# Kernel tuning notes

Measured on AMD Instinct MI355X. Metric: run time of the kernel, lower is better.

Reference implementation:

```python
import jax, jax.numpy as jnp
import numpy as np
import math

B = 8
M = 64
A = 3
NUM_CLASSES = 80
IMG = 608
REDUCTIONS = (8.0, 16.0, 32.0)
XY_SCALES = (1.2, 1.1, 1.05)
IOU_THRESH = 0.213
IGNORE_THRESH = 0.7
COORD_SCALE = 0.07
OBJ_SCALE = 1.0
NOOBJ_SCALE = 1.0
CLASS_SCALE = 1.0
BASE_ANCHORS = np.array([[12,16],[19,36],[40,28],[36,75],[76,55],[72,146],[142,110],[192,243],[459,401]], np.float32)
MASKS = [[0,1,2],[3,4,5],[6,7,8]]
ANCHORS = [jnp.asarray(BASE_ANCHORS[m] / r) for m, r in zip(MASKS, REDUCTIONS)]


def _softplus(x):
    return jnp.logaddexp(x, 0.0)


def _bce_logits(x, t):
    # == sum-reduction BCELoss(sigmoid(x), t), elementwise (stable logits form)
    return _softplus(x) - x * t


def _corners(b):
    x1 = b[..., 0] - b[..., 2] * 0.5
    y1 = b[..., 1] - b[..., 3] * 0.5
    x2 = b[..., 0] + b[..., 2] * 0.5
    y2 = b[..., 1] + b[..., 3] * 0.5
    return x1, y1, x2, y2


def _iou_plain(b1, b2):
    # broadcastable xywh boxes -> plain IoU (matches YOLOLoss.iou with iou_type='iou')
    b1x1, b1y1, b1x2, b1y2 = _corners(b1)
    b2x1, b2y1, b2x2, b2y2 = _corners(b2)
    inter = jnp.clip(jnp.minimum(b1x2, b2x2) - jnp.maximum(b1x1, b2x1), 0) * \
            jnp.clip(jnp.minimum(b1y2, b2y2) - jnp.maximum(b1y1, b2y1), 0)
    union = b1[..., 2] * b1[..., 3] + b2[..., 2] * b2[..., 3] + 1e-16 - inter
    return inter / union


def _ciou(b1, b2):
    # elementwise CIoU (matches YOLOLoss.iou_loss with iou_type='ciou')
    b1x1, b1y1, b1x2, b1y2 = _corners(b1)
    b2x1, b2y1, b2x2, b2y2 = _corners(b2)
    inter = jnp.clip(jnp.minimum(b1x2, b2x2) - jnp.maximum(b1x1, b2x1), 0) * \
            jnp.clip(jnp.minimum(b1y2, b2y2) - jnp.maximum(b1y1, b2y1), 0)
    union = b1[..., 2] * b1[..., 3] + b2[..., 2] * b2[..., 3] + 1e-16 - inter
    iou = inter / union
    cw = jnp.maximum(b1x2, b2x2) - jnp.minimum(b1x1, b2x1)
    ch = jnp.maximum(b1y2, b2y2) - jnp.minimum(b1y1, b2y1)
    c2 = cw ** 2 + ch ** 2 + 1e-16
    rho2 = (b1[..., 0] - b2[..., 0]) ** 2 + (b1[..., 1] - b2[..., 1]) ** 2
    v = (4.0 / math.pi ** 2) * (jnp.arctan(b2[..., 2] / b2[..., 3]) - jnp.arctan(b1[..., 2] / b1[..., 3])) ** 2
    alpha = jax.lax.stop_gradient(v / (1.0 - iou + v + 1e-16))
    return iou - (rho2 / c2 + v * alpha)


def _level_loss(pred, targets, cats, anchor, reduction, xy_scale):
    b, c, h, w = pred.shape
    p = pred.reshape(b, A, NUM_CLASSES + 5, h, w).transpose(0, 1, 3, 4, 2)  # [B,A,H,W,85]
    box_xy = jax.nn.sigmoid(p[..., :2]) * xy_scale - 0.5 * (xy_scale - 1.0)
    box_wh = jnp.exp(p[..., 2:4]) * anchor[None, :, None, None, :]
    obj_logit = p[..., 4]
    cls_logit = p[..., 5:]

    tb = targets[:, :4] / reduction           # [M,4] x1y1x2y2 in grid units
    t_bid = targets[:, 4].astype(jnp.int32)   # image index per target
    wh = tb[:, 2:] - tb[:, :2]                # [M,2]

    # wh_iou anchor<->target matching; match = (iou > thresh) | one_hot(best_anchor)
    a_area = anchor[:, 0] * anchor[:, 1]
    t_area = wh[:, 0] * wh[:, 1]
    inter = jnp.minimum(anchor[:, 0][:, None], wh[:, 0][None, :]) * \
            jnp.minimum(anchor[:, 1][:, None], wh[:, 1][None, :])
    iou_at = inter / (a_area[:, None] + t_area[None, :] - inter)   # [A,M]
    best = jnp.argmax(iou_at, axis=0)                              # [M]
    match = (iou_at > IOU_THRESH) | (jnp.arange(A)[:, None] == best[None, :])  # [A,M]
    matchT = match.T.astype(pred.dtype)                            # [M,A]

    cxcy = (tb[:, :2] + tb[:, 2:]) * 0.5
    ij = cxcy.astype(jnp.int32)
    txy = cxcy - ij.astype(pred.dtype)
    ti, tj = ij[:, 0], ij[:, 1]
    tbox = jnp.concatenate([txy, wh], axis=1)                      # [M,4]

    bI = t_bid[:, None]
    aI = jnp.arange(A)[None, :]
    jI = tj[:, None]
    iI = ti[:, None]
    g_box = jnp.concatenate([box_xy[bI, aI, jI, iI], box_wh[bI, aI, jI, iI]], -1)  # [M,A,4]

    ciou = _ciou(g_box, tbox[:, None, :])                          # [M,A]
    iou_loss = jnp.sum(matchT * (1.0 - ciou)) * COORD_SCALE

    # full decoded boxes with grid offsets (square grids: ys=row, xs=col as in source)
    gx = jnp.arange(w, dtype=pred.dtype)[None, :]
    gy = jnp.arange(h, dtype=pred.dtype)[:, None]
    full_box = jnp.stack([box_xy[..., 0] + gx, box_xy[..., 1] + gy,
                          box_wh[..., 0], box_wh[..., 1]], axis=-1)  # [B,A,H,W,4]

    t_xywh = jnp.concatenate([cxcy, wh], axis=1)                   # [M,4]
    iou_full = _iou_plain(full_box[..., None, :], t_xywh)          # [B,A,H,W,M]
    valid = t_bid[None, None, None, None, :] == jnp.arange(b)[:, None, None, None, None]
    ignore = jnp.any((iou_full > IGNORE_THRESH) & valid, axis=-1)  # [B,A,H,W]
    neg = jnp.where(ignore, 0.0, 1.0).astype(pred.dtype)
    neg = neg.at[bI, aI, jI, iI].min(jnp.where(match.T, 0.0, 1.0).astype(pred.dtype))

    g_obj = obj_logit[bI, aI, jI, iI]                              # [M,A]
    obj_pos = jnp.sum(matchT * _bce_logits(g_obj, 1.0))
    obj_neg = jnp.sum(neg * _softplus(obj_logit))
    obj_loss = OBJ_SCALE * obj_pos + NOOBJ_SCALE * obj_neg

    g_cls = cls_logit[bI, aI, jI, iI]                              # [M,A,nc]
    onehot = jax.nn.one_hot(cats - 1, NUM_CLASSES, dtype=pred.dtype)  # [M,nc]
    cls_loss = jnp.sum(matchT * jnp.sum(_bce_logits(g_cls, onehot[:, None, :]), -1)) * CLASS_SCALE

    return iou_loss, obj_loss, cls_loss


def setup_inputs() -> dict:
    key = jax.random.key(0)
    k = jax.random.split(key, 9)
    pred0 = jax.random.normal(k[0], (B, A * (NUM_CLASSES + 5), 76, 76), jnp.float32)
    pred1 = jax.random.normal(k[1], (B, A * (NUM_CLASSES + 5), 38, 38), jnp.float32)
    pred2 = jax.random.normal(k[2], (B, A * (NUM_CLASSES + 5), 19, 19), jnp.float32)
    cx = jax.random.uniform(k[3], (M,), jnp.float32, 16.0, 592.0)
    cy = jax.random.uniform(k[4], (M,), jnp.float32, 16.0, 592.0)
    bw = jax.random.uniform(k[5], (M,), jnp.float32, 8.0, 120.0)
    bh = jax.random.uniform(k[6], (M,), jnp.float32, 8.0, 120.0)
    bid = jax.random.randint(k[7], (M,), 0, B).astype(jnp.float32)
    targets = jnp.stack([cx - bw * 0.5, cy - bh * 0.5, cx + bw * 0.5, cy + bh * 0.5, bid], axis=1)
    cats = jax.random.randint(k[8], (M,), 1, NUM_CLASSES + 1, jnp.int32)
    return {"pred0": pred0, "pred1": pred1, "pred2": pred2, "targets": targets, "cats": cats}


def reference(pred0, pred1, pred2, targets, cats):
    iou_l = obj_l = cls_l = 0.0
    for pred, anchor, red, xys in zip((pred0, pred1, pred2), ANCHORS, REDUCTIONS, XY_SCALES):
        il, ol, cl = _level_loss(pred, targets, cats, anchor, red, xys)
        iou_l = iou_l + il
        obj_l = obj_l + ol
        cls_l = cls_l + cl
    return jnp.stack([iou_l, obj_l, cls_l])  # (iou_loss, obj_loss, cls_loss)
```

## Files before the change

kernel.cpp:

```cpp
#include <hip/hip_runtime.h>
#include <math.h>

#define NCLS 80
#define NA   3
#define NT   64
#define NB   8


__device__ __forceinline__ float sigm(float x) {
    return __builtin_amdgcn_rcpf(1.f + __expf(-x));
}
__device__ __forceinline__ float softplus_f(float x) {
    return fmaxf(x, 0.f) + __logf(1.f + __expf(-fabsf(x)));
}

template <int LVL>
__device__ __forceinline__ void lvl_consts(float& invred, float& xys, float& bias,
                                           float (&aw)[3], float (&ah)[3]) {
    if (LVL == 0) {
        invred = 0.125f;   xys = 1.2f;
        aw[0] = 1.5f;    aw[1] = 2.375f; aw[2] = 5.0f;
        ah[0] = 2.0f;    ah[1] = 4.5f;   ah[2] = 3.5f;
    } else if (LVL == 1) {
        invred = 0.0625f;  xys = 1.1f;
        aw[0] = 2.25f;   aw[1] = 4.75f;  aw[2] = 4.5f;
        ah[0] = 4.6875f; ah[1] = 3.4375f;ah[2] = 9.125f;
    } else {
        invred = 0.03125f; xys = 1.05f;
        aw[0] = 4.4375f; aw[1] = 6.0f;   aw[2] = 14.34375f;
        ah[0] = 3.4375f; ah[1] = 7.59375f; ah[2] = 12.53125f;
    }
    bias = 0.5f * (xys - 1.f);
}

template <int LVL>
__device__ __forceinline__ void load_target(const float* __restrict__ tgt, int t,
                                            float& x1, float& y1, float& x2, float& y2,
                                            float& w, float& h, float& cx, float& cy,
                                            int& ti, int& tj, int& bid, int& mask) {
    float invred, xys, bias, aw[3], ah[3];
    lvl_consts<LVL>(invred, xys, bias, aw, ah);
    x1 = tgt[t * 5 + 0] * invred;
    y1 = tgt[t * 5 + 1] * invred;
    x2 = tgt[t * 5 + 2] * invred;
    y2 = tgt[t * 5 + 3] * invred;
    bid = (int)tgt[t * 5 + 4];
    w = x2 - x1; h = y2 - y1;
    cx = (x1 + x2) * 0.5f; cy = (y1 + y2) * 0.5f;
    ti = (int)cx; tj = (int)cy;
    float ta = w * h;
    float iou[3];
#pragma unroll
    for (int a = 0; a < 3; a++) {
        float inter = fminf(aw[a], w) * fminf(ah[a], h);
        iou[a] = inter / (aw[a] * ah[a] + ta - inter);
    }
    int best = 0;
    if (iou[1] > iou[best]) best = 1;
    if (iou[2] > iou[best]) best = 2;
    mask = 0;
#pragma unroll
    for (int a = 0; a < 3; a++)
        if (iou[a] > 0.213f || a == best) mask |= (1 << a);
}

template <int LVL, int H, int W>
__device__ void gather_block(const float* __restrict__ pred, const float* __restrict__ tgt,
                             const int* __restrict__ cats, float* __restrict__ out,
                             int g, float* __restrict__ red) {
    const int tid = threadIdx.x;
    const int t0 = g * 4;
    const int HW = H * W;
    float iou_term = 0.f, obj_term = 0.f, cls_term = 0.f;

    for (int u = tid; u < 4 * NA * NCLS; u += 256) {
        int pp = u / NCLS;
        int c  = u - pp * NCLS;
        int t  = t0 + pp / NA;
        int a  = pp - (pp / NA) * NA;
        float x1, y1, x2, y2, w, h, cx, cy;
        int ti, tj, bid, mask;
        load_target<LVL>(tgt, t, x1, y1, x2, y2, w, h, cx, cy, ti, tj, bid, mask);
        if ((mask >> a) & 1) {
            const float* p = pred + (size_t)((bid * NA + a) * (NCLS + 5)) * HW + tj * W + ti;
            float x = p[(size_t)(5 + c) * HW];
            cls_term += softplus_f(x) - ((c == cats[t] - 1) ? x : 0.f);
        }
    }

    if (tid < 4 * NA) {
        int t = t0 + tid / NA, a = tid - (tid / NA) * NA;
        float x1, y1, x2, y2, w, h, cx, cy;
        int ti, tj, bid, mask;
        load_target<LVL>(tgt, t, x1, y1, x2, y2, w, h, cx, cy, ti, tj, bid, mask);
        if ((mask >> a) & 1) {
            float invred, xys, bias, aw[3], ah[3];
            lvl_consts<LVL>(invred, xys, bias, aw, ah);
            const float* p = pred + (size_t)((bid * NA + a) * (NCLS + 5)) * HW + tj * W + ti;
            float q0 = p[0], q1 = p[(size_t)HW], q2 = p[2 * (size_t)HW],
                  q3 = p[3 * (size_t)HW], q4 = p[4 * (size_t)HW];
            float awa = (a == 0) ? aw[0] : ((a == 1) ? aw[1] : aw[2]);
            float aha = (a == 0) ? ah[0] : ((a == 1) ? ah[1] : ah[2]);
            float bx = sigm(q0) * xys - bias;
            float by = sigm(q1) * xys - bias;
            float bw = __expf(q2) * awa;
            float bh = __expf(q3) * aha;
            float tx = cx - (float)ti, ty = cy - (float)tj;

            float b1x1 = bx - bw * 0.5f, b1x2 = bx + bw * 0.5f;
            float b1y1 = by - bh * 0.5f, b1y2 = by + bh * 0.5f;
            float b2x1 = tx - w * 0.5f,  b2x2 = tx + w * 0.5f;
            float b2y1 = ty - h * 0.5f,  b2y2 = ty + h * 0.5f;
            float iw = fmaxf(fminf(b1x2, b2x2) - fmaxf(b1x1, b2x1), 0.f);
            float ih = fmaxf(fminf(b1y2, b2y2) - fmaxf(b1y1, b2y1), 0.f);
            float inter = iw * ih;
            float uni = bw * bh + w * h + 1e-16f - inter;
            float iou = inter / uni;
            float cw  = fmaxf(b1x2, b2x2) - fminf(b1x1, b2x1);
            float chh = fmaxf(b1y2, b2y2) - fminf(b1y1, b2y1);
            float c2 = cw * cw + chh * chh + 1e-16f;
            float rho2 = (bx - tx) * (bx - tx) + (by - ty) * (by - ty);
            float da = atanf(w / h) - atanf(bw / bh);
            float v = 0.4052847345693511f * da * da;
            float alpha = v / (1.f - iou + v + 1e-16f);
            float ciou = iou - (rho2 / c2 + v * alpha);

            iou_term = (1.f - ciou) * 0.07f;
            obj_term = softplus_f(q4) - q4;
        }
    }

#pragma unroll
    for (int off = 32; off > 0; off >>= 1) {
        iou_term += __shfl_down(iou_term, off, 64);
        obj_term += __shfl_down(obj_term, off, 64);
        cls_term += __shfl_down(cls_term, off, 64);
    }
    int lane = tid & 63, wv = tid >> 6;
    if (lane == 0) {
        red[wv * 3 + 0] = iou_term;
        red[wv * 3 + 1] = obj_term;
        red[wv * 3 + 2] = cls_term;
    }
    __syncthreads();
    if (tid == 0) {
        atomicAdd(out + 0, red[0] + red[3] + red[6] + red[9]);
        atomicAdd(out + 1, red[1] + red[4] + red[7] + red[10]);
        atomicAdd(out + 2, red[2] + red[5] + red[8] + red[11]);
    }
}

template <int LVL, int H, int W, int CB>
__device__ void neg_level(const float* __restrict__ pred, const float* __restrict__ tgt,
                          float* __restrict__ out, int blk,
                          float4* eC, float4* eM, int* cnt, float* red) {
    const int tid = threadIdx.x;
    const int b = blk / CB;
    const int cell = (blk - b * CB) * 256 + tid;

    if (tid < 64) {
        float x1, y1, x2, y2, w, h, cx, cy;
        int ti, tj, bid, mask;
        load_target<LVL>(tgt, tid, x1, y1, x2, y2, w, h, cx, cy, ti, tj, bid, mask);
        bool m = (bid == b);
        unsigned long long bal = __ballot(m);
        if (m) {
            int s = (int)__popcll(bal & ((1ull << tid) - 1ull));
            eC[s] = make_float4(x1, y1, x2, y2);
            eM[s] = make_float4(w * h, __int_as_float(ti), __int_as_float(tj),
                                __int_as_float(mask));
        }
        if (tid == 0) *cnt = (int)__popcll(bal);
    }
    __syncthreads();

    const int HW = H * W;
    float contrib = 0.f;
    if (cell < NA * HW) {
        int a = cell / HW;
        int r = cell - a * HW;
        int j = r / W;
        int i = r - j * W;
        float invred, xys, bias, aw[3], ah[3];
        lvl_consts<LVL>(invred, xys, bias, aw, ah);
        const float* p = pred + (size_t)((b * NA + a) * (NCLS + 5)) * HW + r;
        float q0 = p[0], q1 = p[(size_t)HW], q2 = p[2 * (size_t)HW],
              q3 = p[3 * (size_t)HW], q4 = p[4 * (size_t)HW];
        float awa = (a == 0) ? aw[0] : ((a == 1) ? aw[1] : aw[2]);
        float aha = (a == 0) ? ah[0] : ((a == 1) ? ah[1] : ah[2]);
        float bx = sigm(q0) * xys - bias + (float)i;
        float by = sigm(q1) * xys - bias + (float)j;
        float bw = __expf(q2) * awa;
        float bh = __expf(q3) * aha;
        float bx1 = bx - bw * 0.5f, bx2 = bx + bw * 0.5f;
        float by1 = by - bh * 0.5f, by2 = by + bh * 0.5f;
        float barea = bw * bh;

        bool kill = false;
        int n = *cnt;
        for (int k = 0; k < n; k++) {
            float4 c = eC[k];
            float4 m = eM[k];
            float iw = fmaxf(fminf(bx2, c.z) - fmaxf(bx1, c.x), 0.f);
            float ih = fmaxf(fminf(by2, c.w) - fmaxf(by1, c.y), 0.f);
            float inter = iw * ih;
            float uni = barea + m.x + 1e-16f - inter;
            bool ign = inter > 0.7f * uni;
            bool pos = ((__float_as_int(m.w) >> a) & 1) &&
                       (__float_as_int(m.y) == i) && (__float_as_int(m.z) == j);
            kill = kill || ign || pos;
        }
        if (!kill) contrib = softplus_f(q4);
    }

#pragma unroll
    for (int off = 32; off > 0; off >>= 1) contrib += __shfl_down(contrib, off, 64);
    int lane = tid & 63, wv = tid >> 6;
    if (lane == 0) red[wv] = contrib;
    __syncthreads();
    if (tid == 0) atomicAdd(out + 1, red[0] + red[1] + red[2] + red[3]);
}

__global__ __launch_bounds__(256) void yolo_loss_kernel(
        const float* __restrict__ p0, const float* __restrict__ p1,
        const float* __restrict__ p2, const float* __restrict__ tgt,
        const int* __restrict__ cats, float* __restrict__ out) {
    __shared__ float4 eC[NT];
    __shared__ float4 eM[NT];
    __shared__ int cnt;
    __shared__ float red[12];
    int blk = blockIdx.x;
    if (blk < 544)       neg_level<0, 76, 76, 68>(p0, tgt, out, blk,       eC, eM, &cnt, red);
    else if (blk < 680)  neg_level<1, 38, 38, 17>(p1, tgt, out, blk - 544, eC, eM, &cnt, red);
    else if (blk < 720)  neg_level<2, 19, 19, 5 >(p2, tgt, out, blk - 680, eC, eM, &cnt, red);
    else if (blk < 736)  gather_block<0, 76, 76>(p0, tgt, cats, out, blk - 720, red);
    else if (blk < 752)  gather_block<1, 38, 38>(p1, tgt, cats, out, blk - 736, red);
    else                 gather_block<2, 19, 19>(p2, tgt, cats, out, blk - 752, red);
}

extern "C" void kernel_launch(void* const* d_in, const int* in_sizes, int n_in,
                              void* d_out, int out_size, void* d_ws, size_t ws_size,
                              hipStream_t stream) {
    const float* p0   = (const float*)d_in[0];
    const float* p1   = (const float*)d_in[1];
    const float* p2   = (const float*)d_in[2];
    const float* tgt  = (const float*)d_in[3];
    const int*   cats = (const int*)d_in[4];
    float* out = (float*)d_out;

    yolo_loss_kernel<<<768, 256, 0, stream>>>(p0, p1, p2, tgt, cats, out);
}
```

Measured before the change: 102.0 us.

## Process four cells per thread with float4 loads in negative objectness pass

Levels 0 and 1 of the negative-objectness pass now have each thread handle four consecutive cells. It loads them with float4 vector loads and tests all four against each shared target in one inner loop. This cuts the block count from 768 to 264 and amortises the per-block target setup and shared-memory target reads. The gather block also computes per-target descriptors (offset, class, validity) once into shared memory, instead of recomputing load_target for every class element. In exchange, fewer blocks means less parallelism across the GPU, and per-thread register use goes up.

```diff
diff --git a/kernel.cpp b/kernel.cpp
--- a/kernel.cpp
+++ b/kernel.cpp
@@ -64,90 +64,100 @@
         if (iou[a] > 0.213f || a == best) mask |= (1 << a);
 }
 
-template <int LVL, int H, int W>
-__device__ void gather_block(const float* __restrict__ pred, const float* __restrict__ tgt,
-                             const int* __restrict__ cats, float* __restrict__ out,
-                             int g, float* __restrict__ red) {
+struct GatherDesc { long off; int cat; int valid; };
+
+template <int LVL, int H, int W, int CB>
+__device__ void neg_level_quad(const float* __restrict__ pred, const float* __restrict__ tgt,
+                               float* __restrict__ out, int blk,
+                               float4* eC, float4* eM, int* cnt, float* red) {
     const int tid = threadIdx.x;
-    const int t0 = g * 4;
+    const int b = blk / CB;
+    const int q = (blk - b * CB) * 256 + tid;
     const int HW = H * W;
-    float iou_term = 0.f, obj_term = 0.f, cls_term = 0.f;
-
-    for (int u = tid; u < 4 * NA * NCLS; u += 256) {
-        int pp = u / NCLS;
-        int c  = u - pp * NCLS;
-        int t  = t0 + pp / NA;
-        int a  = pp - (pp / NA) * NA;
+    const int QUADS = NA * HW / 4;
+
+    if (tid < 64) {
         float x1, y1, x2, y2, w, h, cx, cy;
         int ti, tj, bid, mask;
-        load_target<LVL>(tgt, t, x1, y1, x2, y2, w, h, cx, cy, ti, tj, bid, mask);
-        if ((mask >> a) & 1) {
-            const float* p = pred + (size_t)((bid * NA + a) * (NCLS + 5)) * HW + tj * W + ti;
-            float x = p[(size_t)(5 + c) * HW];
-            cls_term += softplus_f(x) - ((c == cats[t] - 1) ? x : 0.f);
-        }
-    }
-
-    if (tid < 4 * NA) {
-        int t = t0 + tid / NA, a = tid - (tid / NA) * NA;
-        float x1, y1, x2, y2, w, h, cx, cy;
-        int ti, tj, bid, mask;
-        load_target<LVL>(tgt, t, x1, y1, x2, y2, w, h, cx, cy, ti, tj, bid, mask);
-        if ((mask >> a) & 1) {
-            float invred, xys, bias, aw[3], ah[3];
-            lvl_consts<LVL>(invred, xys, bias, aw, ah);
-            const float* p = pred + (size_t)((bid * NA + a) * (NCLS + 5)) * HW + tj * W + ti;
-            float q0 = p[0], q1 = p[(size_t)HW], q2 = p[2 * (size_t)HW],
-                  q3 = p[3 * (size_t)HW], q4 = p[4 * (size_t)HW];
-            float awa = (a == 0) ? aw[0] : ((a == 1) ? aw[1] : aw[2]);
-            float aha = (a == 0) ? ah[0] : ((a == 1) ? ah[1] : ah[2]);
-            float bx = sigm(q0) * xys - bias;
-            float by = sigm(q1) * xys - bias;
-            float bw = __expf(q2) * awa;
-            float bh = __expf(q3) * aha;
-            float tx = cx - (float)ti, ty = cy - (float)tj;
-
-            float b1x1 = bx - bw * 0.5f, b1x2 = bx + bw * 0.5f;
-            float b1y1 = by - bh * 0.5f, b1y2 = by + bh * 0.5f;
-            float b2x1 = tx - w * 0.5f,  b2x2 = tx + w * 0.5f;
-            float b2y1 = ty - h * 0.5f,  b2y2 = ty + h * 0.5f;
-            float iw = fmaxf(fminf(b1x2, b2x2) - fmaxf(b1x1, b2x1), 0.f);
-            float ih = fmaxf(fminf(b1y2, b2y2) - fmaxf(b1y1, b2y1), 0.f);
-            float inter = iw * ih;
-            float uni = bw * bh + w * h + 1e-16f - inter;
-            float iou = inter / uni;
-            float cw  = fmaxf(b1x2, b2x2) - fminf(b1x1, b2x1);
-            float chh = fmaxf(b1y2, b2y2) - fminf(b1y1, b2y1);
-            float c2 = cw * cw + chh * chh + 1e-16f;
-            float rho2 = (bx - tx) * (bx - tx) + (by - ty) * (by - ty);
-            float da = atanf(w / h) - atanf(bw / bh);
-            float v = 0.4052847345693511f * da * da;
-            float alpha = v / (1.f - iou + v + 1e-16f);
-            float ciou = iou - (rho2 / c2 + v * alpha);
-
-            iou_term = (1.f - ciou) * 0.07f;
-            obj_term = softplus_f(q4) - q4;
-        }
-    }
-
-#pragma unroll
-    for (int off = 32; off > 0; off >>= 1) {
-        iou_term += __shfl_down(iou_term, off, 64);
-        obj_term += __shfl_down(obj_term, off, 64);
-        cls_term += __shfl_down(cls_term, off, 64);
-    }
+        load_target<LVL>(tgt, tid, x1, y1, x2, y2, w, h, cx, cy, ti, tj, bid, mask);
+        bool m = (bid == b);
+        unsigned long long bal = __ballot(m);
+        if (m) {
+            int s = (int)__popcll(bal & ((1ull << tid) - 1ull));
+            eC[s] = make_float4(x1, y1, x2, y2);
+            eM[s] = make_float4(w * h, __int_as_float(ti), __int_as_float(tj),
+                                __int_as_float(mask));
+        }
+        if (tid == 0) *cnt = (int)__popcll(bal);
+    }
+    __syncthreads();
+
+    float contrib = 0.f;
+    if (q < QUADS) {
+        const int cell = q * 4;
+        const int a = cell / HW;
+        const int r = cell - a * HW;
+        float invred, xys, bias, aw[3], ah[3];
+        lvl_consts<LVL>(invred, xys, bias, aw, ah);
+        const float* p = pred + (size_t)((b * NA + a) * (NCLS + 5)) * HW + r;
+        float4 v0 = *(const float4*)p;
+        float4 v1 = *(const float4*)(p + (size_t)HW);
+        float4 v2 = *(const float4*)(p + 2 * (size_t)HW);
+        float4 v3 = *(const float4*)(p + 3 * (size_t)HW);
+        float4 v4 = *(const float4*)(p + 4 * (size_t)HW);
+        float awa = (a == 0) ? aw[0] : ((a == 1) ? aw[1] : aw[2]);
+        float aha = (a == 0) ? ah[0] : ((a == 1) ? ah[1] : ah[2]);
+
+        float bx1[4], bx2[4], by1[4], by2[4], bar[4], q4s[4];
+        int   ii[4], jj[4];
+#pragma unroll
+        for (int e = 0; e < 4; e++) {
+            int rr = r + e;
+            int j = rr / W, i = rr - j * W;
+            ii[e] = i; jj[e] = j;
+            float s0 = ((const float*)&v0)[e];
+            float s1 = ((const float*)&v1)[e];
+            float s2 = ((const float*)&v2)[e];
+            float s3 = ((const float*)&v3)[e];
+            q4s[e]   = ((const float*)&v4)[e];
+            float bx = sigm(s0) * xys - bias + (float)i;
+            float by = sigm(s1) * xys - bias + (float)j;
+            float bw = __expf(s2) * awa;
+            float bh = __expf(s3) * aha;
+            bx1[e] = bx - bw * 0.5f; bx2[e] = bx + bw * 0.5f;
+            by1[e] = by - bh * 0.5f; by2[e] = by + bh * 0.5f;
+            bar[e] = bw * bh;
+        }
+
+        int killm = 0;
+        const int n = *cnt;
+        for (int k = 0; k < n; k++) {
+            float4 c = eC[k];
+            float4 m = eM[k];
+            int mi = __float_as_int(m.y), mj = __float_as_int(m.z);
+            int mk = __float_as_int(m.w);
+#pragma unroll
+            for (int e = 0; e < 4; e++) {
+                float iw = fmaxf(fminf(bx2[e], c.z) - fmaxf(bx1[e], c.x), 0.f);
+                float ih = fmaxf(fminf(by2[e], c.w) - fmaxf(by1[e], c.y), 0.f);
+                float inter = iw * ih;
+                float uni = bar[e] + m.x + 1e-16f - inter;
+                bool ign = inter > 0.7f * uni;
+                bool pos = ((mk >> a) & 1) && (mi == ii[e]) && (mj == jj[e]);
+                if (ign || pos) killm |= (1 << e);
+            }
+        }
+#pragma unroll
+        for (int e = 0; e < 4; e++)
+            if (!((killm >> e) & 1)) contrib += softplus_f(q4s[e]);
+    }
+
+#pragma unroll
+    for (int off = 32; off > 0; off >>= 1) contrib += __shfl_down(contrib, off, 64);
     int lane = tid & 63, wv = tid >> 6;
-    if (lane == 0) {
-        red[wv * 3 + 0] = iou_term;
-        red[wv * 3 + 1] = obj_term;
-        red[wv * 3 + 2] = cls_term;
-    }
-    __syncthreads();
-    if (tid == 0) {
-        atomicAdd(out + 0, red[0] + red[3] + red[6] + red[9]);
-        atomicAdd(out + 1, red[1] + red[4] + red[7] + red[10]);
-        atomicAdd(out + 2, red[2] + red[5] + red[8] + red[11]);
-    }
+    if (lane == 0) red[wv] = contrib;
+    __syncthreads();
+    if (tid == 0) atomicAdd(out + 1, red[0] + red[1] + red[2] + red[3]);
 }
 
 template <int LVL, int H, int W, int CB>
@@ -221,6 +231,92 @@
     if (tid == 0) atomicAdd(out + 1, red[0] + red[1] + red[2] + red[3]);
 }
 
+template <int LVL, int H, int W>
+__device__ void gather_block(const float* __restrict__ pred, const float* __restrict__ tgt,
+                             const int* __restrict__ cats, float* __restrict__ out,
+                             int g, GatherDesc* gd, float* __restrict__ red) {
+    const int tid = threadIdx.x;
+    const int t0 = g * 4;
+    const int HW = H * W;
+    float iou_term = 0.f, obj_term = 0.f, cls_term = 0.f;
+
+    if (tid < 4 * NA) {
+        int t = t0 + tid / NA, a = tid - (tid / NA) * NA;
+        float x1, y1, x2, y2, w, h, cx, cy;
+        int ti, tj, bid, mask;
+        load_target<LVL>(tgt, t, x1, y1, x2, y2, w, h, cx, cy, ti, tj, bid, mask);
+        int valid = (mask >> a) & 1;
+        long off = (long)((bid * NA + a) * (NCLS + 5)) * HW + tj * W + ti;
+        gd[tid].off = off;
+        gd[tid].cat = cats[t] - 1;
+        gd[tid].valid = valid;
+        if (valid) {
+            float invred, xys, bias, aw[3], ah[3];
+            lvl_consts<LVL>(invred, xys, bias, aw, ah);
+            const float* p = pred + off;
+            float q0 = p[0], q1 = p[(size_t)HW], q2 = p[2 * (size_t)HW],
+                  q3 = p[3 * (size_t)HW], q4 = p[4 * (size_t)HW];
+            float awa = (a == 0) ? aw[0] : ((a == 1) ? aw[1] : aw[2]);
+            float aha = (a == 0) ? ah[0] : ((a == 1) ? ah[1] : ah[2]);
+            float bx = sigm(q0) * xys - bias;
+            float by = sigm(q1) * xys - bias;
+            float bw = __expf(q2) * awa;
+            float bh = __expf(q3) * aha;
+            float tx = cx - (float)ti, ty = cy - (float)tj;
+
+            float b1x1 = bx - bw * 0.5f, b1x2 = bx + bw * 0.5f;
+            float b1y1 = by - bh * 0.5f, b1y2 = by + bh * 0.5f;
+            float b2x1 = tx - w * 0.5f,  b2x2 = tx + w * 0.5f;
+            float b2y1 = ty - h * 0.5f,  b2y2 = ty + h * 0.5f;
+            float iw = fmaxf(fminf(b1x2, b2x2) - fmaxf(b1x1, b2x1), 0.f);
+            float ih = fmaxf(fminf(b1y2, b2y2) - fmaxf(b1y1, b2y1), 0.f);
+            float inter = iw * ih;
+            float uni = bw * bh + w * h + 1e-16f - inter;
+            float iou = inter / uni;
+            float cw  = fmaxf(b1x2, b2x2) - fminf(b1x1, b2x1);
+            float chh = fmaxf(b1y2, b2y2) - fminf(b1y1, b2y1);
+            float c2 = cw * cw + chh * chh + 1e-16f;
+            float rho2 = (bx - tx) * (bx - tx) + (by - ty) * (by - ty);
+            float da = atanf(w / h) - atanf(bw / bh);
+            float v = 0.4052847345693511f * da * da;
+            float alpha = v / (1.f - iou + v + 1e-16f);
+            float ciou = iou - (rho2 / c2 + v * alpha);
+
+            iou_term = (1.f - ciou) * 0.07f;
+            obj_term = softplus_f(q4) - q4;
+        }
+    }
+    __syncthreads();
+
+    for (int u = tid; u < 4 * NA * NCLS; u += 256) {
+        int pp = u / NCLS;
+        int c  = u - pp * NCLS;
+        if (gd[pp].valid) {
+            float x = pred[gd[pp].off + (long)(5 + c) * HW];
+            cls_term += softplus_f(x) - ((c == gd[pp].cat) ? x : 0.f);
+        }
+    }
+
+#pragma unroll
+    for (int off = 32; off > 0; off >>= 1) {
+        iou_term += __shfl_down(iou_term, off, 64);
+        obj_term += __shfl_down(obj_term, off, 64);
+        cls_term += __shfl_down(cls_term, off, 64);
+    }
+    int lane = tid & 63, wv = tid >> 6;
+    if (lane == 0) {
+        red[wv * 3 + 0] = iou_term;
+        red[wv * 3 + 1] = obj_term;
+        red[wv * 3 + 2] = cls_term;
+    }
+    __syncthreads();
+    if (tid == 0) {
+        atomicAdd(out + 0, red[0] + red[3] + red[6] + red[9]);
+        atomicAdd(out + 1, red[1] + red[4] + red[7] + red[10]);
+        atomicAdd(out + 2, red[2] + red[5] + red[8] + red[11]);
+    }
+}
+
 __global__ __launch_bounds__(256) void yolo_loss_kernel(
         const float* __restrict__ p0, const float* __restrict__ p1,
         const float* __restrict__ p2, const float* __restrict__ tgt,
@@ -229,13 +325,14 @@
     __shared__ float4 eM[NT];
     __shared__ int cnt;
     __shared__ float red[12];
+    __shared__ GatherDesc gd[12];
     int blk = blockIdx.x;
-    if (blk < 544)       neg_level<0, 76, 76, 68>(p0, tgt, out, blk,       eC, eM, &cnt, red);
-    else if (blk < 680)  neg_level<1, 38, 38, 17>(p1, tgt, out, blk - 544, eC, eM, &cnt, red);
-    else if (blk < 720)  neg_level<2, 19, 19, 5 >(p2, tgt, out, blk - 680, eC, eM, &cnt, red);
-    else if (blk < 736)  gather_block<0, 76, 76>(p0, tgt, cats, out, blk - 720, red);
-    else if (blk < 752)  gather_block<1, 38, 38>(p1, tgt, cats, out, blk - 736, red);
-    else                 gather_block<2, 19, 19>(p2, tgt, cats, out, blk - 752, red);
+    if (blk < 136)       neg_level_quad<0, 76, 76, 17>(p0, tgt, out, blk,       eC, eM, &cnt, red);
+    else if (blk < 176)  neg_level_quad<1, 38, 38, 5 >(p1, tgt, out, blk - 136, eC, eM, &cnt, red);
+    else if (blk < 216)  neg_level<2, 19, 19, 5>(p2, tgt, out, blk - 176, eC, eM, &cnt, red);
+    else if (blk < 232)  gather_block<0, 76, 76>(p0, tgt, cats, out, blk - 216, gd, red);
+    else if (blk < 248)  gather_block<1, 38, 38>(p1, tgt, cats, out, blk - 232, gd, red);
+    else                 gather_block<2, 19, 19>(p2, tgt, cats, out, blk - 248, gd, red);
 }
 
 extern "C" void kernel_launch(void* const* d_in, const int* in_sizes, int n_in,
@@ -248,5 +345,5 @@
     const int*   cats = (const int*)d_in[4];
     float* out = (float*)d_out;
 
-    yolo_loss_kernel<<<768, 256, 0, stream>>>(p0, p1, p2, tgt, cats, out);
-}
+    yolo_loss_kernel<<<264, 256, 0, stream>>>(p0, p1, p2, tgt, cats, out);
+}
```

Result: faster. 95.32 us (-6.5%).
